# Kernel optimization log

Measured on AMD Instinct MI355X. Metric: run time of the kernel, lower is better.

Reference implementation:

```python
import jax, jax.numpy as jnp
import numpy as np

DIM = 768
NUM_HEADS = 12
HEAD_DIM = DIM // NUM_HEADS
SCALE = HEAD_DIM ** -0.5


def setup_inputs() -> dict:
    key = jax.random.key(0)
    ks = jax.random.split(key, 6)
    B, Lq, Lkv = 8, 1024, 1024
    return {
        "q": jax.random.normal(ks[0], (B, Lq, DIM), dtype=jnp.float32),
        "kv": jax.random.normal(ks[1], (B, Lkv, DIM), dtype=jnp.float32),
        "attn_pos": jax.random.normal(ks[2], (1, NUM_HEADS, Lq, Lkv), dtype=jnp.float32),
        "Wq": jax.random.normal(ks[3], (DIM, DIM), dtype=jnp.float32) * (DIM ** -0.5),
        "Wkv": jax.random.normal(ks[4], (2 * DIM, DIM), dtype=jnp.float32) * (DIM ** -0.5),
        "Wproj": jax.random.normal(ks[5], (DIM, DIM), dtype=jnp.float32) * (DIM ** -0.5),
        "bproj": jnp.zeros((DIM,), dtype=jnp.float32),
    }


def reference(q, kv, attn_pos, Wq, Wkv, Wproj, bproj):
    B, Lq, C = q.shape
    Lkv = kv.shape[1]
    H, D = NUM_HEADS, HEAD_DIM
    # q/kv projections (torch Linear: x @ W.T); attn_pos_encoding_only path
    qh = (q @ Wq.T).reshape(B, Lq, H, D).transpose(0, 2, 1, 3)        # (B,H,Lq,D)
    kvp = (kv @ Wkv.T).reshape(B, Lkv, 2, H, D).transpose(2, 0, 3, 1, 4)
    k, v = kvp[0], kvp[1]                                             # (B,H,Lkv,D)
    # scaled dot-product attention with additive positional bias
    attn = jnp.einsum('bhqd,bhkd->bhqk', qh, k) * SCALE + attn_pos    # (B,H,Lq,Lkv)
    attn = jax.nn.softmax(attn, axis=-1)
    x = jnp.einsum('bhqk,bhkd->bhqd', attn, v)                        # (B,H,Lq,D)
    x = x.transpose(0, 2, 1, 3).reshape(B, Lq, C)
    return x @ Wproj.T + bproj
```

## Files before the change

kernel.cpp:

```cpp
#include <hip/hip_runtime.h>

#define DIM 768
#define NHEADS 12
#define HDIM 64
#define BATCH 8
#define LQ 1024
#define LKV 1024
#define ATTN_SCALE 0.125f

typedef __bf16 bf16;
typedef __bf16 bf16x4 __attribute__((ext_vector_type(4)));
typedef __bf16 bf16x8 __attribute__((ext_vector_type(8)));
typedef short s16x4 __attribute__((ext_vector_type(4)));
typedef float f32x4 __attribute__((ext_vector_type(4)));

union B4 { bf16x4 h; s16x4 s; };

static __device__ __forceinline__ f32x4 mfma_k32(bf16x8 a, bf16x8 b, f32x4 c) {
    return __builtin_amdgcn_mfma_f32_16x16x32_bf16(a, b, c, 0, 0, 0);
}
static __device__ __forceinline__ f32x4 mfma_k16(s16x4 a, s16x4 b, f32x4 c) {
    return __builtin_amdgcn_mfma_f32_16x16x16bf16_1k(a, b, c, 0, 0, 0);
}

static __device__ __forceinline__ void async16(const bf16* g, bf16* l) {
    __builtin_amdgcn_global_load_lds(
        (const __attribute__((address_space(1))) unsigned int*)g,
        (__attribute__((address_space(3))) unsigned int*)l, 16, 0, 0);
}
static __device__ __forceinline__ void drain_vmem() {
    __asm__ volatile("s_waitcnt vmcnt(0)" ::: "memory");
}

__global__ void cvt_qkv(const float4* __restrict__ q, const float4* __restrict__ kv,
                        bf16x4* __restrict__ qb, bf16x4* __restrict__ kvb, int n4) {
    int i = blockIdx.x * 256 + threadIdx.x;
    if (i >= n4) return;
    const float4* src = blockIdx.y ? kv : q;
    bf16x4* dst = blockIdx.y ? kvb : qb;
    float4 v = src[i];
    bf16x4 o;
    o[0] = (bf16)v.x; o[1] = (bf16)v.y; o[2] = (bf16)v.z; o[3] = (bf16)v.w;
    dst[i] = o;
}

__global__ void cvt_w(const float4* __restrict__ Wq, const float4* __restrict__ Wkv,
                      const float4* __restrict__ Wp,
                      bf16x4* __restrict__ wall, bf16x4* __restrict__ wpb, int n4) {
    int i = blockIdx.x * 256 + threadIdx.x;
    if (i >= n4) return;
    int y = blockIdx.y;
    const float4* src; bf16x4* dst;
    if (y == 0)      { src = Wq;             dst = wall; }
    else if (y == 3) { src = Wp;             dst = wpb; }
    else             { src = Wkv + (y - 1) * n4; dst = wall + y * n4; }
    float4 v = src[i];
    bf16x4 o;
    o[0] = (bf16)v.x; o[1] = (bf16)v.y; o[2] = (bf16)v.z; o[3] = (bf16)v.w;
    dst[i] = o;
}

__global__ __launch_bounds__(256) void proj_gemm(
    const bf16* __restrict__ qb, const bf16* __restrict__ kvb,
    const bf16* __restrict__ W,
    bf16* __restrict__ Qp, bf16* __restrict__ Kp, bf16* __restrict__ Vt)
{
    __shared__ bf16 As[128 * 32];
    __shared__ bf16 Bs[128 * 32];
    const int tid  = threadIdx.x;
    const int lane = tid & 63;
    const int w    = tid >> 6;
    const int wm = (w >> 1) * 64;
    const int wn = (w & 1) * 64;
    const int m0 = blockIdx.x * 128;
    const int n0 = blockIdx.y * 128;
    const int K = DIM;
    const int lq = lane & 15;
    const int quad = lane >> 4;

    const bf16* A = (n0 < DIM) ? qb : kvb;
    const int isV = (n0 >= 2 * DIM);

    const int rl = lane >> 2;
    const int ck = (lane & 3) * 8;
    const bf16* gA = A + (size_t)(m0 + w * 32 + rl) * K + ck;
    const bf16* gB = W + (size_t)(n0 + w * 32 + rl) * K + ck;
    bf16* lA = &As[w * 1024];
    bf16* lB = &Bs[w * 1024];

    f32x4 acc[4][4] = {};

    for (int k0 = 0; k0 < K; k0 += 32) {
        async16(gA + k0,                  lA);
        async16(gA + (size_t)16 * K + k0, lA + 512);
        async16(gB + k0,                  lB);
        async16(gB + (size_t)16 * K + k0, lB + 512);
        drain_vmem();
        __syncthreads();

        bf16x8 a[4], b[4];
        #pragma unroll
        for (int i = 0; i < 4; i++)
            a[i] = *(const bf16x8*)&As[(wm + i * 16 + lq) * 32 + quad * 8];
        #pragma unroll
        for (int j = 0; j < 4; j++)
            b[j] = *(const bf16x8*)&Bs[(wn + j * 16 + lq) * 32 + quad * 8];
        if (isV) {
            #pragma unroll
            for (int i = 0; i < 4; i++)
                #pragma unroll
                for (int j = 0; j < 4; j++)
                    acc[i][j] = mfma_k32(a[i], b[j], acc[i][j]);
        } else {
            #pragma unroll
            for (int i = 0; i < 4; i++)
                #pragma unroll
                for (int j = 0; j < 4; j++)
                    acc[i][j] = mfma_k32(b[j], a[i], acc[i][j]);
        }
        __syncthreads();
    }

    if (isV) {
        const int n0v = n0 - 2 * DIM;
        #pragma unroll
        for (int i = 0; i < 4; i++) {
            const int base_m = m0 + wm + i * 16;
            const int b_idx = base_m >> 10;
            const int kvl = (base_m & 1023) + quad * 4;
            #pragma unroll
            for (int j = 0; j < 4; j++) {
                const int nl = n0v + wn + j * 16 + lq;
                const int h = nl >> 6;
                const int d = nl & 63;
                B4 pk;
                #pragma unroll
                for (int r = 0; r < 4; r++) pk.h[r] = (bf16)acc[i][j][r];
                *(s16x4*)&Vt[(((size_t)b_idx * NHEADS + h) * HDIM + d) * LKV + kvl] = pk.s;
            }
        }
    } else {
        bf16* Cb = (n0 < DIM) ? Qp : Kp;
        const int nb = (n0 < DIM) ? n0 : n0 - DIM;
        #pragma unroll
        for (int i = 0; i < 4; i++) {
            const size_t row = m0 + wm + i * 16 + lq;
            #pragma unroll
            for (int j = 0; j < 4; j++) {
                const int col = nb + wn + j * 16 + quad * 4;
                B4 pk;
                #pragma unroll
                for (int r = 0; r < 4; r++) pk.h[r] = (bf16)acc[i][j][r];
                *(s16x4*)&Cb[row * DIM + col] = pk.s;
            }
        }
    }
}

__global__ __launch_bounds__(256) void out_gemm(
    const bf16* __restrict__ A, const bf16* __restrict__ B,
    float* __restrict__ Cp, const float* __restrict__ bias, int M, int N, int K)
{
    __shared__ bf16 As[128 * 32];
    __shared__ bf16 Bs[128 * 32];
    const int tid  = threadIdx.x;
    const int lane = tid & 63;
    const int w    = tid >> 6;
    const int wm = (w >> 1) * 64;
    const int wn = (w & 1) * 64;
    const int m0 = blockIdx.x * 128;
    const int n0 = blockIdx.y * 128;
    const int lq = lane & 15;
    const int quad = lane >> 4;

    const int rl = lane >> 2;
    const int ck = (lane & 3) * 8;
    const bf16* gA = A + (size_t)(m0 + w * 32 + rl) * K + ck;
    const bf16* gB = B + (size_t)(n0 + w * 32 + rl) * K + ck;
    bf16* lA = &As[w * 1024];
    bf16* lB = &Bs[w * 1024];

    f32x4 acc[4][4] = {};

    for (int k0 = 0; k0 < K; k0 += 32) {
        async16(gA + k0,                  lA);
        async16(gA + (size_t)16 * K + k0, lA + 512);
        async16(gB + k0,                  lB);
        async16(gB + (size_t)16 * K + k0, lB + 512);
        drain_vmem();
        __syncthreads();

        bf16x8 a[4], b[4];
        #pragma unroll
        for (int i = 0; i < 4; i++)
            a[i] = *(const bf16x8*)&As[(wm + i * 16 + lq) * 32 + quad * 8];
        #pragma unroll
        for (int j = 0; j < 4; j++)
            b[j] = *(const bf16x8*)&Bs[(wn + j * 16 + lq) * 32 + quad * 8];
        #pragma unroll
        for (int i = 0; i < 4; i++)
            #pragma unroll
            for (int j = 0; j < 4; j++)
                acc[i][j] = mfma_k32(b[j], a[i], acc[i][j]);
        __syncthreads();
    }

    #pragma unroll
    for (int i = 0; i < 4; i++) {
        const size_t row = m0 + wm + i * 16 + lq;
        #pragma unroll
        for (int j = 0; j < 4; j++) {
            const int col = n0 + wn + j * 16 + quad * 4;
            float4 bj = *(const float4*)&bias[col];
            float4 o;
            o.x = acc[i][j][0] + bj.x; o.y = acc[i][j][1] + bj.y;
            o.z = acc[i][j][2] + bj.z; o.w = acc[i][j][3] + bj.w;
            *(float4*)&Cp[row * N + col] = o;
        }
    }
}

__global__ __launch_bounds__(256) void attn_kernel(
    const bf16* __restrict__ Qb,
    const bf16* __restrict__ Kb,
    const bf16* __restrict__ Vt,
    const float* __restrict__ pos,
    bf16* __restrict__ O)
{
    __shared__ bf16 Ks[64 * 72];
    __shared__ bf16 Vs[64 * 72];

    const int by = blockIdx.y;
    const int h = by >> 3, b = by & 7;
    const int bh = b * NHEADS + h;
    const int q0 = blockIdx.x * 64;
    const int t = threadIdx.x;
    const int lane = t & 63;
    const int w = t >> 6;
    const int lq = lane & 15;
    const int quad = lane >> 4;

    const bf16* qg = Qb + (size_t)(b * LQ + q0 + w * 16 + lq) * DIM + h * HDIM + quad * 8;
    bf16x8 qa[2];
    qa[0] = *(const bf16x8*)(qg);
    qa[1] = *(const bf16x8*)(qg + 32);

    float m_r = -1e30f, l_r = 0.f;
    f32x4 o_acc[4] = {};

    const float4* pos4 = (const float4*)(pos + ((size_t)h * LQ + q0 + w * 16 + lq) * LKV);

    for (int kv0 = 0; kv0 < LKV; kv0 += 64) {
        #pragma unroll
        for (int p = 0; p < 2; p++) {
            int row = (t >> 3) + p * 32;
            int c8  = (t & 7) * 8;
            *(uint4*)&Ks[row * 72 + c8] =
                *(const uint4*)(Kb + (size_t)(b * LKV + kv0 + row) * DIM + h * HDIM + c8);
            *(uint4*)&Vs[row * 72 + c8] =
                *(const uint4*)(Vt + (size_t)(bh * HDIM + row) * LKV + kv0 + c8);
        }
        __syncthreads();

        float4 pb[4];
        #pragma unroll
        for (int kvblk = 0; kvblk < 4; kvblk++)
            pb[kvblk] = pos4[(kv0 >> 2) + kvblk * 4 + quad];

        f32x4 sc[4];
        #pragma unroll
        for (int kvblk = 0; kvblk < 4; kvblk++) {
            sc[kvblk] = (f32x4){0.f, 0.f, 0.f, 0.f};
            #pragma unroll
            for (int kt = 0; kt < 2; kt++) {
                bf16x8 ak = *(const bf16x8*)&Ks[(kvblk * 16 + lq) * 72 + kt * 32 + quad * 8];
                sc[kvblk] = mfma_k32(ak, qa[kt], sc[kvblk]);
            }
        }

        float sv[4][4];
        #pragma unroll
        for (int kvblk = 0; kvblk < 4; kvblk++) {
            sv[kvblk][0] = sc[kvblk][0] * ATTN_SCALE + pb[kvblk].x;
            sv[kvblk][1] = sc[kvblk][1] * ATTN_SCALE + pb[kvblk].y;
            sv[kvblk][2] = sc[kvblk][2] * ATTN_SCALE + pb[kvblk].z;
            sv[kvblk][3] = sc[kvblk][3] * ATTN_SCALE + pb[kvblk].w;
        }

        float tmax = sv[0][0];
        #pragma unroll
        for (int kvblk = 0; kvblk < 4; kvblk++)
            #pragma unroll
            for (int r = 0; r < 4; r++)
                tmax = fmaxf(tmax, sv[kvblk][r]);
        tmax = fmaxf(tmax, __shfl_xor(tmax, 16));
        tmax = fmaxf(tmax, __shfl_xor(tmax, 32));
        float mn = fmaxf(m_r, tmax);
        float alpha = __expf(m_r - mn);
        float rs = 0.f;
        B4 pfrag[4];
        #pragma unroll
        for (int kvblk = 0; kvblk < 4; kvblk++) {
            #pragma unroll
            for (int r = 0; r < 4; r++) {
                float pv = __expf(sv[kvblk][r] - mn);
                rs += pv;
                pfrag[kvblk].h[r] = (bf16)pv;
            }
        }
        rs += __shfl_xor(rs, 16);
        rs += __shfl_xor(rs, 32);
        l_r = l_r * alpha + rs;
        m_r = mn;

        #pragma unroll
        for (int dblk = 0; dblk < 4; dblk++) {
            o_acc[dblk][0] *= alpha; o_acc[dblk][1] *= alpha;
            o_acc[dblk][2] *= alpha; o_acc[dblk][3] *= alpha;
        }

        #pragma unroll
        for (int dblk = 0; dblk < 4; dblk++) {
            #pragma unroll
            for (int kvblk = 0; kvblk < 4; kvblk++) {
                s16x4 va = *(const s16x4*)&Vs[(dblk * 16 + lq) * 72 + kvblk * 16 + quad * 4];
                o_acc[dblk] = mfma_k16(va, pfrag[kvblk].s, o_acc[dblk]);
            }
        }
        __syncthreads();
    }

    float inv = 1.f / l_r;
    const size_t orow = (size_t)(b * LQ + q0 + w * 16 + lq) * DIM + h * HDIM;
    #pragma unroll
    for (int dblk = 0; dblk < 4; dblk++) {
        B4 ob;
        #pragma unroll
        for (int r = 0; r < 4; r++) ob.h[r] = (bf16)(o_acc[dblk][r] * inv);
        *(s16x4*)&O[orow + dblk * 16 + quad * 4] = ob.s;
    }
}

extern "C" void kernel_launch(void* const* d_in, const int* in_sizes, int n_in,
                              void* d_out, int out_size, void* d_ws, size_t ws_size,
                              hipStream_t stream) {
    const float* q     = (const float*)d_in[0];
    const float* kv    = (const float*)d_in[1];
    const float* pos   = (const float*)d_in[2];
    const float* Wq    = (const float*)d_in[3];
    const float* Wkv   = (const float*)d_in[4];
    const float* Wproj = (const float*)d_in[5];
    const float* bproj = (const float*)d_in[6];
    float* out = (float*)d_out;

    char* ws = (char*)d_ws;
    size_t off = 0;
    auto alloc = [&](size_t bytes) -> void* {
        void* p = ws + off;
        off += (bytes + 255) & ~(size_t)255;
        return p;
    };

    const int M = BATCH * LQ;
    bf16* qb   = (bf16*)alloc((size_t)M * DIM * 2);
    bf16* kvb  = (bf16*)alloc((size_t)M * DIM * 2);
    bf16* wall = (bf16*)alloc((size_t)3 * DIM * DIM * 2);
    bf16* wpb  = (bf16*)alloc((size_t)DIM * DIM * 2);
    bf16* Qp   = (bf16*)alloc((size_t)M * DIM * 2);
    bf16* Kp   = (bf16*)alloc((size_t)M * DIM * 2);
    bf16* Vt   = (bf16*)alloc((size_t)BATCH * NHEADS * HDIM * LKV * 2);
    bf16* Ob   = (bf16*)alloc((size_t)M * DIM * 2);

    {
        int n4 = M * DIM / 4;
        cvt_qkv<<<dim3((n4 + 255) / 256, 2), 256, 0, stream>>>(
            (const float4*)q, (const float4*)kv, (bf16x4*)qb, (bf16x4*)kvb, n4);
        int w4 = DIM * DIM / 4;
        cvt_w<<<dim3((w4 + 255) / 256, 4), 256, 0, stream>>>(
            (const float4*)Wq, (const float4*)Wkv, (const float4*)Wproj,
            (bf16x4*)wall, (bf16x4*)wpb, w4);
    }

    proj_gemm<<<dim3(M / 128, (3 * DIM) / 128), 256, 0, stream>>>(qb, kvb, wall, Qp, Kp, Vt);
    attn_kernel<<<dim3(LQ / 64, NHEADS * BATCH), 256, 0, stream>>>(Qp, Kp, Vt, pos, Ob);
    out_gemm<<<dim3(M / 128, DIM / 128), 256, 0, stream>>>(Ob, wpb, out, bproj, M, DIM, DIM);
}
```

Baseline: 299.5 us.

## Double-buffer GEMM and attention tiles, merge conversion kernels, shrink out_gemm tile

Adds double-buffered LDS staging to proj_gemm, out_gemm and the attention kernel, so the loads for the next K/V or K-slice tile are issued while MFMAs run on the current one. In attention, the next tile is held in registers and written to the other buffer after compute. The two fp32-to-bf16 conversion kernels become one launch. out_gemm moves to 64x128 tiles to double its block count and improve CU occupancy. The cost is twice the LDS per block and more live registers, which may lower occupancy.

```diff
diff --git a/kernel.cpp b/kernel.cpp
--- a/kernel.cpp
+++ b/kernel.cpp
@@ -32,32 +32,25 @@
     __asm__ volatile("s_waitcnt vmcnt(0)" ::: "memory");
 }
 
-__global__ void cvt_qkv(const float4* __restrict__ q, const float4* __restrict__ kv,
-                        bf16x4* __restrict__ qb, bf16x4* __restrict__ kvb, int n4) {
+#define NQ4 (BATCH * LQ * DIM / 4)
+#define NW4 (DIM * DIM / 4)
+__global__ void cvt_all(const float4* __restrict__ q, const float4* __restrict__ kv,
+                        const float4* __restrict__ Wq, const float4* __restrict__ Wkv,
+                        const float4* __restrict__ Wp,
+                        bf16x4* __restrict__ qb, bf16x4* __restrict__ kvb,
+                        bf16x4* __restrict__ wall, bf16x4* __restrict__ wpb) {
     int i = blockIdx.x * 256 + threadIdx.x;
-    if (i >= n4) return;
-    const float4* src = blockIdx.y ? kv : q;
-    bf16x4* dst = blockIdx.y ? kvb : qb;
-    float4 v = src[i];
+    const float4* src; bf16x4* dst; int j;
+    if (i < NQ4)                { src = q;   dst = qb;        j = i; }
+    else if (i < 2 * NQ4)       { src = kv;  dst = kvb;       j = i - NQ4; }
+    else if (i < 2 * NQ4 + NW4) { src = Wq;  dst = wall;      j = i - 2 * NQ4; }
+    else if (i < 2 * NQ4 + 3 * NW4) { src = Wkv; dst = wall + NW4; j = i - 2 * NQ4 - NW4; }
+    else if (i < 2 * NQ4 + 4 * NW4) { src = Wp;  dst = wpb;   j = i - 2 * NQ4 - 3 * NW4; }
+    else return;
+    float4 v = src[j];
     bf16x4 o;
     o[0] = (bf16)v.x; o[1] = (bf16)v.y; o[2] = (bf16)v.z; o[3] = (bf16)v.w;
-    dst[i] = o;
-}
-
-__global__ void cvt_w(const float4* __restrict__ Wq, const float4* __restrict__ Wkv,
-                      const float4* __restrict__ Wp,
-                      bf16x4* __restrict__ wall, bf16x4* __restrict__ wpb, int n4) {
-    int i = blockIdx.x * 256 + threadIdx.x;
-    if (i >= n4) return;
-    int y = blockIdx.y;
-    const float4* src; bf16x4* dst;
-    if (y == 0)      { src = Wq;             dst = wall; }
-    else if (y == 3) { src = Wp;             dst = wpb; }
-    else             { src = Wkv + (y - 1) * n4; dst = wall + y * n4; }
-    float4 v = src[i];
-    bf16x4 o;
-    o[0] = (bf16)v.x; o[1] = (bf16)v.y; o[2] = (bf16)v.z; o[3] = (bf16)v.w;
-    dst[i] = o;
+    dst[j] = o;
 }
 
 __global__ __launch_bounds__(256) void proj_gemm(
@@ -65,8 +58,8 @@
     const bf16* __restrict__ W,
     bf16* __restrict__ Qp, bf16* __restrict__ Kp, bf16* __restrict__ Vt)
 {
-    __shared__ bf16 As[128 * 32];
-    __shared__ bf16 Bs[128 * 32];
+    __shared__ bf16 As[2 * 128 * 32];
+    __shared__ bf16 Bs[2 * 128 * 32];
     const int tid  = threadIdx.x;
     const int lane = tid & 63;
     const int w    = tid >> 6;
@@ -85,26 +78,40 @@
     const int ck = (lane & 3) * 8;
     const bf16* gA = A + (size_t)(m0 + w * 32 + rl) * K + ck;
     const bf16* gB = W + (size_t)(n0 + w * 32 + rl) * K + ck;
-    bf16* lA = &As[w * 1024];
-    bf16* lB = &Bs[w * 1024];
 
     f32x4 acc[4][4] = {};
 
-    for (int k0 = 0; k0 < K; k0 += 32) {
-        async16(gA + k0,                  lA);
-        async16(gA + (size_t)16 * K + k0, lA + 512);
-        async16(gB + k0,                  lB);
-        async16(gB + (size_t)16 * K + k0, lB + 512);
+    {
+        bf16* lA = &As[w * 1024];
+        bf16* lB = &Bs[w * 1024];
+        async16(gA,                  lA);
+        async16(gA + (size_t)16 * K, lA + 512);
+        async16(gB,                  lB);
+        async16(gB + (size_t)16 * K, lB + 512);
         drain_vmem();
         __syncthreads();
-
+    }
+
+    int cur = 0;
+    for (int k0 = 0; k0 < K; k0 += 32) {
+        const int nxt = k0 + 32;
+        if (nxt < K) {
+            bf16* lA = &As[(cur ^ 1) * 4096 + w * 1024];
+            bf16* lB = &Bs[(cur ^ 1) * 4096 + w * 1024];
+            async16(gA + nxt,                  lA);
+            async16(gA + (size_t)16 * K + nxt, lA + 512);
+            async16(gB + nxt,                  lB);
+            async16(gB + (size_t)16 * K + nxt, lB + 512);
+        }
+        const bf16* Ab = &As[cur * 4096];
+        const bf16* Bb = &Bs[cur * 4096];
         bf16x8 a[4], b[4];
         #pragma unroll
         for (int i = 0; i < 4; i++)
-            a[i] = *(const bf16x8*)&As[(wm + i * 16 + lq) * 32 + quad * 8];
+            a[i] = *(const bf16x8*)&Ab[(wm + i * 16 + lq) * 32 + quad * 8];
         #pragma unroll
         for (int j = 0; j < 4; j++)
-            b[j] = *(const bf16x8*)&Bs[(wn + j * 16 + lq) * 32 + quad * 8];
+            b[j] = *(const bf16x8*)&Bb[(wn + j * 16 + lq) * 32 + quad * 8];
         if (isV) {
             #pragma unroll
             for (int i = 0; i < 4; i++)
@@ -118,7 +125,9 @@
                 for (int j = 0; j < 4; j++)
                     acc[i][j] = mfma_k32(b[j], a[i], acc[i][j]);
         }
+        drain_vmem();
         __syncthreads();
+        cur ^= 1;
     }
 
     if (isV) {
@@ -161,52 +170,66 @@
     const bf16* __restrict__ A, const bf16* __restrict__ B,
     float* __restrict__ Cp, const float* __restrict__ bias, int M, int N, int K)
 {
-    __shared__ bf16 As[128 * 32];
-    __shared__ bf16 Bs[128 * 32];
+    __shared__ bf16 As[2 * 64 * 32];
+    __shared__ bf16 Bs[2 * 128 * 32];
     const int tid  = threadIdx.x;
     const int lane = tid & 63;
     const int w    = tid >> 6;
-    const int wm = (w >> 1) * 64;
+    const int wm = (w >> 1) * 32;
     const int wn = (w & 1) * 64;
-    const int m0 = blockIdx.x * 128;
+    const int m0 = blockIdx.x * 64;
     const int n0 = blockIdx.y * 128;
     const int lq = lane & 15;
     const int quad = lane >> 4;
 
     const int rl = lane >> 2;
     const int ck = (lane & 3) * 8;
-    const bf16* gA = A + (size_t)(m0 + w * 32 + rl) * K + ck;
+    const bf16* gA = A + (size_t)(m0 + w * 16 + rl) * K + ck;
     const bf16* gB = B + (size_t)(n0 + w * 32 + rl) * K + ck;
-    bf16* lA = &As[w * 1024];
-    bf16* lB = &Bs[w * 1024];
-
-    f32x4 acc[4][4] = {};
-
-    for (int k0 = 0; k0 < K; k0 += 32) {
-        async16(gA + k0,                  lA);
-        async16(gA + (size_t)16 * K + k0, lA + 512);
-        async16(gB + k0,                  lB);
-        async16(gB + (size_t)16 * K + k0, lB + 512);
+
+    f32x4 acc[2][4] = {};
+
+    {
+        bf16* lA = &As[w * 512];
+        bf16* lB = &Bs[w * 1024];
+        async16(gA,                  lA);
+        async16(gB,                  lB);
+        async16(gB + (size_t)16 * K, lB + 512);
         drain_vmem();
         __syncthreads();
-
-        bf16x8 a[4], b[4];
-        #pragma unroll
-        for (int i = 0; i < 4; i++)
-            a[i] = *(const bf16x8*)&As[(wm + i * 16 + lq) * 32 + quad * 8];
+    }
+
+    int cur = 0;
+    for (int k0 = 0; k0 < K; k0 += 32) {
+        const int nxt = k0 + 32;
+        if (nxt < K) {
+            bf16* lA = &As[(cur ^ 1) * 2048 + w * 512];
+            bf16* lB = &Bs[(cur ^ 1) * 4096 + w * 1024];
+            async16(gA + nxt,                  lA);
+            async16(gB + nxt,                  lB);
+            async16(gB + (size_t)16 * K + nxt, lB + 512);
+        }
+        const bf16* Ab = &As[cur * 2048];
+        const bf16* Bb = &Bs[cur * 4096];
+        bf16x8 a[2], b[4];
+        #pragma unroll
+        for (int i = 0; i < 2; i++)
+            a[i] = *(const bf16x8*)&Ab[(wm + i * 16 + lq) * 32 + quad * 8];
         #pragma unroll
         for (int j = 0; j < 4; j++)
-            b[j] = *(const bf16x8*)&Bs[(wn + j * 16 + lq) * 32 + quad * 8];
-        #pragma unroll
-        for (int i = 0; i < 4; i++)
+            b[j] = *(const bf16x8*)&Bb[(wn + j * 16 + lq) * 32 + quad * 8];
+        #pragma unroll
+        for (int i = 0; i < 2; i++)
             #pragma unroll
             for (int j = 0; j < 4; j++)
                 acc[i][j] = mfma_k32(b[j], a[i], acc[i][j]);
+        drain_vmem();
         __syncthreads();
+        cur ^= 1;
     }
 
     #pragma unroll
-    for (int i = 0; i < 4; i++) {
+    for (int i = 0; i < 2; i++) {
         const size_t row = m0 + wm + i * 16 + lq;
         #pragma unroll
         for (int j = 0; j < 4; j++) {
@@ -227,8 +250,8 @@
     const float* __restrict__ pos,
     bf16* __restrict__ O)
 {
-    __shared__ bf16 Ks[64 * 72];
-    __shared__ bf16 Vs[64 * 72];
+    __shared__ bf16 Ks[2 * 64 * 72];
+    __shared__ bf16 Vs[2 * 64 * 72];
 
     const int by = blockIdx.y;
     const int h = by >> 3, b = by & 7;
@@ -240,27 +263,46 @@
     const int lq = lane & 15;
     const int quad = lane >> 4;
 
+    const int srow = t >> 3;
+    const int sc8  = (t & 7) * 8;
+    const bf16* gK = Kb + (size_t)(b * LKV + srow) * DIM + h * HDIM + sc8;
+    const bf16* gV = Vt + (size_t)(bh * HDIM + srow) * LKV + sc8;
+
     const bf16* qg = Qb + (size_t)(b * LQ + q0 + w * 16 + lq) * DIM + h * HDIM + quad * 8;
     bf16x8 qa[2];
     qa[0] = *(const bf16x8*)(qg);
     qa[1] = *(const bf16x8*)(qg + 32);
 
+    {
+        uint4 k0r = *(const uint4*)(gK);
+        uint4 k1r = *(const uint4*)(gK + (size_t)32 * DIM);
+        uint4 v0r = *(const uint4*)(gV);
+        uint4 v1r = *(const uint4*)(gV + (size_t)32 * LKV);
+        *(uint4*)&Ks[srow * 72 + sc8]        = k0r;
+        *(uint4*)&Ks[(srow + 32) * 72 + sc8] = k1r;
+        *(uint4*)&Vs[srow * 72 + sc8]        = v0r;
+        *(uint4*)&Vs[(srow + 32) * 72 + sc8] = v1r;
+    }
+    __syncthreads();
+
     float m_r = -1e30f, l_r = 0.f;
     f32x4 o_acc[4] = {};
 
     const float4* pos4 = (const float4*)(pos + ((size_t)h * LQ + q0 + w * 16 + lq) * LKV);
 
+    int cur = 0;
     for (int kv0 = 0; kv0 < LKV; kv0 += 64) {
-        #pragma unroll
-        for (int p = 0; p < 2; p++) {
-            int row = (t >> 3) + p * 32;
-            int c8  = (t & 7) * 8;
-            *(uint4*)&Ks[row * 72 + c8] =
-                *(const uint4*)(Kb + (size_t)(b * LKV + kv0 + row) * DIM + h * HDIM + c8);
-            *(uint4*)&Vs[row * 72 + c8] =
-                *(const uint4*)(Vt + (size_t)(bh * HDIM + row) * LKV + kv0 + c8);
-        }
-        __syncthreads();
+        const int nxt = kv0 + 64;
+        uint4 k0r, k1r, v0r, v1r;
+        if (nxt < LKV) {
+            k0r = *(const uint4*)(gK + (size_t)nxt * DIM);
+            k1r = *(const uint4*)(gK + (size_t)(nxt + 32) * DIM);
+            v0r = *(const uint4*)(gV + nxt);
+            v1r = *(const uint4*)(gV + (size_t)32 * LKV + nxt);
+        }
+
+        const bf16* Kc = &Ks[cur * 4608];
+        const bf16* Vc = &Vs[cur * 4608];
 
         float4 pb[4];
         #pragma unroll
@@ -273,7 +315,7 @@
             sc[kvblk] = (f32x4){0.f, 0.f, 0.f, 0.f};
             #pragma unroll
             for (int kt = 0; kt < 2; kt++) {
-                bf16x8 ak = *(const bf16x8*)&Ks[(kvblk * 16 + lq) * 72 + kt * 32 + quad * 8];
+                bf16x8 ak = *(const bf16x8*)&Kc[(kvblk * 16 + lq) * 72 + kt * 32 + quad * 8];
                 sc[kvblk] = mfma_k32(ak, qa[kt], sc[kvblk]);
             }
         }
@@ -323,11 +365,21 @@
         for (int dblk = 0; dblk < 4; dblk++) {
             #pragma unroll
             for (int kvblk = 0; kvblk < 4; kvblk++) {
-                s16x4 va = *(const s16x4*)&Vs[(dblk * 16 + lq) * 72 + kvblk * 16 + quad * 4];
+                s16x4 va = *(const s16x4*)&Vc[(dblk * 16 + lq) * 72 + kvblk * 16 + quad * 4];
                 o_acc[dblk] = mfma_k16(va, pfrag[kvblk].s, o_acc[dblk]);
             }
         }
+
+        if (nxt < LKV) {
+            bf16* Kn = &Ks[(cur ^ 1) * 4608];
+            bf16* Vn = &Vs[(cur ^ 1) * 4608];
+            *(uint4*)&Kn[srow * 72 + sc8]        = k0r;
+            *(uint4*)&Kn[(srow + 32) * 72 + sc8] = k1r;
+            *(uint4*)&Vn[srow * 72 + sc8]        = v0r;
+            *(uint4*)&Vn[(srow + 32) * 72 + sc8] = v1r;
+        }
         __syncthreads();
+        cur ^= 1;
     }
 
     float inv = 1.f / l_r;
@@ -372,16 +424,14 @@
     bf16* Ob   = (bf16*)alloc((size_t)M * DIM * 2);
 
     {
-        int n4 = M * DIM / 4;
-        cvt_qkv<<<dim3((n4 + 255) / 256, 2), 256, 0, stream>>>(
-            (const float4*)q, (const float4*)kv, (bf16x4*)qb, (bf16x4*)kvb, n4);
-        int w4 = DIM * DIM / 4;
-        cvt_w<<<dim3((w4 + 255) / 256, 4), 256, 0, stream>>>(
-            (const float4*)Wq, (const float4*)Wkv, (const float4*)Wproj,
-            (bf16x4*)wall, (bf16x4*)wpb, w4);
+        int total = 2 * NQ4 + 4 * NW4;
+        cvt_all<<<(total + 255) / 256, 256, 0, stream>>>(
+            (const float4*)q, (const float4*)kv, (const float4*)Wq,
+            (const float4*)Wkv, (const float4*)Wproj,
+            (bf16x4*)qb, (bf16x4*)kvb, (bf16x4*)wall, (bf16x4*)wpb);
     }
 
     proj_gemm<<<dim3(M / 128, (3 * DIM) / 128), 256, 0, stream>>>(qb, kvb, wall, Qp, Kp, Vt);
     attn_kernel<<<dim3(LQ / 64, NHEADS * BATCH), 256, 0, stream>>>(Qp, Kp, Vt, pos, Ob);
-    out_gemm<<<dim3(M / 128, DIM / 128), 256, 0, stream>>>(Ob, wpb, out, bproj, M, DIM, DIM);
-}
+    out_gemm<<<dim3(M / 64, DIM / 128), 256, 0, stream>>>(Ob, wpb, out, bproj, M, DIM, DIM);
+}
```

After: 316.1 us. 1.06x slower.
